# Kernel optimization log

Hardware: AMD Instinct MI355X
Metric: run time of the kernel (lower is better)

The kernel has to match this reference:

```python
import jax, jax.numpy as jnp
import numpy as np

N, E, F = 32768, 131072, 32

# (l_in, l_edge, l_out, op_type) for each of the 12 active paths; index = row of W
PATHS = [
    (0, 0, 0, 'prod'), (0, 1, 1, 'prod'), (0, 2, 2, 'prod'),
    (1, 0, 1, 'prod'), (2, 0, 2, 'prod'),
    (1, 1, 0, 'dot'), (1, 1, 1, 'cross'), (1, 1, 2, 'outer'),
    (2, 1, 1, 'mat_vec'), (1, 2, 1, 'vec_mat'),
    (2, 2, 0, 'double_dot'), (2, 2, 2, 'mat_mul_sym'),
]


def setup_inputs() -> dict:
    key = jax.random.key(0)
    ks = jax.random.split(key, 8)
    return {
        'h0': jax.random.normal(ks[0], (N, F), jnp.float32),
        'h1': jax.random.normal(ks[1], (N, 3, F), jnp.float32),
        'h2': jax.random.normal(ks[2], (N, 3, 3, F), jnp.float32),
        'g0': jax.random.normal(ks[3], (E, F), jnp.float32),
        'g1': jax.random.normal(ks[4], (E, 3, F), jnp.float32),
        'g2': jax.random.normal(ks[5], (E, 3, 3, F), jnp.float32),
        'W': jax.random.normal(ks[6], (len(PATHS), F, F), jnp.float32) * (F ** -0.5),
        'src': jax.random.randint(ks[7], (E,), 0, N, jnp.int32).astype(jnp.int64),
    }


def _leibniz(h0, h1, h2, g0, g1, g2, W, src):
    inv_sqrt_f = h0.shape[-1] ** -0.5
    # gather source-node features once per l
    h = {0: h0[src], 1: h1[src], 2: h2[src]}
    g = {0: g0, 1: g1, 2: g2}
    eye = jnp.eye(3, dtype=h0.dtype)[None, :, :, None]  # [1,3,3,1]
    msgs = {0: [], 1: [], 2: []}
    for p, (li, le, lo, op) in enumerate(PATHS):
        # nn.Linear(F,F,bias=False): y = x @ W^T, applied on last (feature) axis
        ht = jnp.einsum('...f,gf->...g', h[li], W[p])
        geom = g[le]
        if op == 'prod':
            if li == 0 and le == 0:
                res = ht * geom
            elif li == 0 and le == 1:
                res = ht[:, None, :] * geom
            elif li == 0 and le == 2:
                res = ht[:, None, None, :] * geom
            elif li == 1 and le == 0:
                res = ht * geom[:, None, :]
            else:  # li == 2, le == 0
                res = ht * geom[:, None, None, :]
        elif op == 'dot':
            res = jnp.sum(ht * geom, axis=1)
        elif op == 'cross':
            res = jnp.cross(ht, geom, axisa=1, axisb=1, axisc=1)
        elif op == 'outer':
            outer = ht[:, :, None, :] * geom[:, None, :, :]  # [E,3,3,F]
            trace = jnp.einsum('eiif->ef', outer)
            res = outer - (1.0 / 3.0) * trace[:, None, None, :] * eye
        elif op == 'mat_vec':
            res = jnp.einsum('eijf,ejf->eif', ht, geom)
        elif op == 'vec_mat':
            res = jnp.einsum('eif,eijf->ejf', ht, geom)
        elif op == 'double_dot':
            res = jnp.sum(ht * geom, axis=(1, 2))
        else:  # mat_mul_sym
            raw = jnp.einsum('eikf,ekjf->eijf', ht, geom)
            sym = 0.5 * (raw + jnp.swapaxes(raw, 1, 2))
            trace = jnp.einsum('eiif->ef', sym)
            res = sym - (1.0 / 3.0) * trace[:, None, None, :] * eye
        msgs[lo].append(res * inv_sqrt_f)
    return tuple(sum(msgs[l]) for l in (0, 1, 2))


def reference(h0, h1, h2, g0, g1, g2, W, src):
    return _leibniz(h0, h1, h2, g0, g1, g2, W, src)
```

## Files before the change

kernel.cpp:

```cpp
#include <hip/hip_runtime.h>

typedef float f32x4 __attribute__((ext_vector_type(4)));
typedef __bf16 bf16x8 __attribute__((ext_vector_type(8)));
typedef __bf16 bf16x4 __attribute__((ext_vector_type(4)));

constexpr float INV_SQRT_F = 0.17677669529663687f;

__device__ __forceinline__ f32x4 mfma16(bf16x8 a, bf16x8 b) {
  const f32x4 z = {0.f, 0.f, 0.f, 0.f};
  return __builtin_amdgcn_mfma_f32_16x16x32_bf16(a, b, z, 0, 0, 0);
}
__device__ __forceinline__ f32x4 ld4(const float* p) {
  return *reinterpret_cast<const f32x4*>(p);
}
__device__ __forceinline__ bf16x8 ldb8(const __bf16* __restrict__ p) {
  return *reinterpret_cast<const bf16x8*>(p);
}
__device__ __forceinline__ bf16x8 cvt_frag(f32x4 u, f32x4 v) {
  bf16x8 r;
  r[0] = (__bf16)u[0]; r[1] = (__bf16)u[1]; r[2] = (__bf16)u[2]; r[3] = (__bf16)u[3];
  r[4] = (__bf16)v[0]; r[5] = (__bf16)v[1]; r[6] = (__bf16)v[2]; r[7] = (__bf16)v[3];
  return r;
}

__global__ __launch_bounds__(256)
void leibniz_prepass(const float* __restrict__ h0, const float* __restrict__ h1,
                     const float* __restrict__ h2, const float* __restrict__ Wg,
                     __bf16* __restrict__ ws, int n0, int n1, int n2)
{
  if (blockIdx.x == 0) {
    bf16x8* wsW = reinterpret_cast<bf16x8*>(ws);
    for (int c = threadIdx.x; c < 12 * 2 * 4 * 16; c += 256) {
      const int gl = c & 15;
      const int qq = (c >> 4) & 3;
      const int hf = (c >> 6) & 1;
      const int p  = c >> 7;
      const float* wp = Wg + (p * 32 + hf * 16 + gl) * 32 + qq * 8;
      bf16x8 f;
#pragma unroll
      for (int j = 0; j < 8; ++j) f[j] = (__bf16)(wp[j] * INV_SQRT_F);
      wsW[c] = f;
    }
  }
  __bf16* hb0 = ws + 12288;
  __bf16* hb1 = hb0 + n0;
  __bf16* hb2 = hb1 + n1;
  const int q0 = n0 >> 2, q1 = n1 >> 2, q2 = n2 >> 2;
  const int total = q0 + q1 + q2;
  for (int i = blockIdx.x * 256 + threadIdx.x; i < total; i += gridDim.x * 256) {
    const float* sp;
    __bf16* dp;
    if (i < q0)           { sp = h0 + 4 * i;              dp = hb0 + 4 * i; }
    else if (i < q0 + q1) { int j = i - q0;      sp = h1 + 4 * j; dp = hb1 + 4 * j; }
    else                  { int j = i - q0 - q1; sp = h2 + 4 * j; dp = hb2 + 4 * j; }
    const f32x4 v = *reinterpret_cast<const f32x4*>(sp);
    bf16x4 o;
    o[0] = (__bf16)v[0]; o[1] = (__bf16)v[1]; o[2] = (__bf16)v[2]; o[3] = (__bf16)v[3];
    *reinterpret_cast<bf16x4*>(dp) = o;
  }
}

__global__ __launch_bounds__(256, 2)
void leibniz_half(const __bf16* __restrict__ wsAll,
                  const float* __restrict__ g0, const float* __restrict__ g1,
                  const float* __restrict__ g2, const int* __restrict__ src,
                  float* __restrict__ out, int E, int n0, int n1)
{
  __shared__ bf16x8 wlds[12 * 2 * 4 * 16];
  {
    const bf16x8* wsW = reinterpret_cast<const bf16x8*>(wsAll);
    for (int c = threadIdx.x; c < 12 * 2 * 4 * 16; c += 256) wlds[c] = wsW[c];
  }
  __syncthreads();

  const __bf16* hb0 = wsAll + 12288;
  const __bf16* hb1 = hb0 + n0;
  const __bf16* hb2 = hb1 + n1;

  const int lane = threadIdx.x & 63;
  const int wid  = threadIdx.x >> 6;
  const int half = wid & 1;
  const int tile = wid >> 1;
  const int eidx = lane & 15;
  const int q    = lane >> 4;
  int e0 = (blockIdx.x * 2 + tile) * 16;
  if (e0 > E - 16) e0 = E - 16;

  const int node = src[e0 + eidx];
  const int e    = e0 + eidx;
  const int col  = q * 4 + 16 * half;

  const float* g0p = g0 + (long long)e * 32 + col;
  const float* g1p = g1 + (long long)e * 96 + col;
  const float* g2p = g2 + (long long)e * 288 + col;
  const f32x4 gv0 = ld4(g0p);
  f32x4 gv1[3];
#pragma unroll
  for (int s = 0; s < 3; ++s) gv1[s] = ld4(g1p + s * 32);
  f32x4 gk[9];
#pragma unroll
  for (int s = 0; s < 9; ++s) gk[s] = ld4(g2p + s * 32);

  const int k0 = q * 8;
  const bf16x8 b0 = ldb8(hb0 + (long long)node * 32 + k0);
  bf16x8 b1[3];
#pragma unroll
  for (int s = 0; s < 3; ++s) b1[s] = ldb8(hb1 + (long long)node * 96 + s * 32 + k0);
  bf16x8 b2[9];
#pragma unroll
  for (int s = 0; s < 9; ++s) b2[s] = ldb8(hb2 + (long long)node * 288 + s * 32 + k0);

#define WFRAG(P) (wlds[(((P) * 2 + half) * 4 + q) * 16 + eidx])

  f32x4 acc0 = mfma16(WFRAG(0), b0) * gv0;
  f32x4 acc1[3];
  f32x4 acc2[9];
  {
    const bf16x8 w3 = WFRAG(3);
#pragma unroll
    for (int s = 0; s < 3; ++s) acc1[s] = mfma16(w3, b1[s]) * gv0;
    const bf16x8 w4 = WFRAG(4);
#pragma unroll
    for (int s = 0; s < 9; ++s) acc2[s] = mfma16(w4, b2[s]) * gv0;
  }

  {
    const f32x4 t = mfma16(WFRAG(1), b0);
#pragma unroll
    for (int s = 0; s < 3; ++s) acc1[s] += t * gv1[s];
  }
  {
    const bf16x8 w5 = WFRAG(5);
#pragma unroll
    for (int s = 0; s < 3; ++s) acc0 += mfma16(w5, b1[s]) * gv1[s];
  }
  {
    const bf16x8 w6 = WFRAG(6);
    const f32x4 c0 = mfma16(w6, b1[0]);
    const f32x4 c1 = mfma16(w6, b1[1]);
    const f32x4 c2 = mfma16(w6, b1[2]);
    acc1[0] += c1 * gv1[2] - c2 * gv1[1];
    acc1[1] += c2 * gv1[0] - c0 * gv1[2];
    acc1[2] += c0 * gv1[1] - c1 * gv1[0];
  }
  {
    const bf16x8 w7 = WFRAG(7);
    const f32x4 o0 = mfma16(w7, b1[0]);
    const f32x4 o1 = mfma16(w7, b1[1]);
    const f32x4 o2 = mfma16(w7, b1[2]);
    const f32x4 tr3 = (o0 * gv1[0] + o1 * gv1[1] + o2 * gv1[2]) * (1.f / 3.f);
    acc2[0] += o0 * gv1[0] - tr3;
    acc2[1] += o0 * gv1[1];
    acc2[2] += o0 * gv1[2];
    acc2[3] += o1 * gv1[0];
    acc2[4] += o1 * gv1[1] - tr3;
    acc2[5] += o1 * gv1[2];
    acc2[6] += o2 * gv1[0];
    acc2[7] += o2 * gv1[1];
    acc2[8] += o2 * gv1[2] - tr3;
  }
  {
    const bf16x8 w8 = WFRAG(8);
#pragma unroll
    for (int a = 0; a < 3; ++a)
#pragma unroll
      for (int b = 0; b < 3; ++b)
        acc1[a] += mfma16(w8, b2[a * 3 + b]) * gv1[b];
  }

  {
    const f32x4 t2 = mfma16(WFRAG(2), b0);
#pragma unroll
    for (int ss = 0; ss < 9; ++ss) acc2[ss] += t2 * gk[ss];
  }
  {
    const bf16x8 w9 = WFRAG(9);
#pragma unroll
    for (int i = 0; i < 3; ++i) {
      const f32x4 vk = mfma16(w9, b1[i]);
#pragma unroll
      for (int j = 0; j < 3; ++j) acc1[j] += vk * gk[i * 3 + j];
    }
  }
  {
    const bf16x8 w10 = WFRAG(10);
#pragma unroll
    for (int ss = 0; ss < 9; ++ss) acc0 += mfma16(w10, b2[ss]) * gk[ss];
  }
  {
    const bf16x8 w11 = WFRAG(11);
#pragma unroll
    for (int k = 0; k < 3; ++k) {
      const f32x4 m0 = mfma16(w11, b2[0 * 3 + k]);
      const f32x4 m1 = mfma16(w11, b2[1 * 3 + k]);
      const f32x4 m2 = mfma16(w11, b2[2 * 3 + k]);
      const f32x4 gk0 = gk[k * 3 + 0];
      const f32x4 gk1 = gk[k * 3 + 1];
      const f32x4 gk2 = gk[k * 3 + 2];
      const f32x4 tk3 = (m0 * gk0 + m1 * gk1 + m2 * gk2) * (1.f / 3.f);
      acc2[0] += m0 * gk0 - tk3;
      acc2[4] += m1 * gk1 - tk3;
      acc2[8] += m2 * gk2 - tk3;
      const f32x4 s01 = (m0 * gk1 + m1 * gk0) * 0.5f;
      acc2[1] += s01; acc2[3] += s01;
      const f32x4 s02 = (m0 * gk2 + m2 * gk0) * 0.5f;
      acc2[2] += s02; acc2[6] += s02;
      const f32x4 s12 = (m1 * gk2 + m2 * gk1) * 0.5f;
      acc2[5] += s12; acc2[7] += s12;
    }
  }

  __builtin_amdgcn_s_barrier();

  float* o0p = out + (long long)e * 32 + col;
  float* o1p = out + (long long)E * 32 + (long long)e * 96 + col;
  float* o2p = out + (long long)E * 128 + (long long)e * 288 + col;
  *reinterpret_cast<f32x4*>(o0p) = acc0;
#pragma unroll
  for (int s = 0; s < 3; ++s) *reinterpret_cast<f32x4*>(o1p + s * 32) = acc1[s];
#pragma unroll
  for (int s = 0; s < 9; ++s) *reinterpret_cast<f32x4*>(o2p + s * 32) = acc2[s];
#undef WFRAG
}

__device__ __forceinline__ bf16x8 load_frag8(const float* __restrict__ p) {
  return cvt_frag(ld4(p), ld4(p + 4));
}
__device__ __forceinline__ f32x4 ntload4(const float* __restrict__ p) {
  return __builtin_nontemporal_load(reinterpret_cast<const f32x4*>(p));
}
__device__ __forceinline__ void ntstore4(float* __restrict__ p, f32x4 v) {
  __builtin_nontemporal_store(v, reinterpret_cast<f32x4*>(p));
}

__global__ __launch_bounds__(256, 2)
void leibniz_fused(const float* __restrict__ h0, const float* __restrict__ h1,
                   const float* __restrict__ h2, const float* __restrict__ g0,
                   const float* __restrict__ g1, const float* __restrict__ g2,
                   const float* __restrict__ Wg, const int* __restrict__ src,
                   float* __restrict__ out, int E)
{
  __shared__ bf16x8 wlds[12 * 2 * 4 * 16];
  for (int c = threadIdx.x; c < 12 * 2 * 4 * 16; c += 256) {
    const int gl = c & 15;
    const int qq = (c >> 4) & 3;
    const int hf = (c >> 6) & 1;
    const int p  = c >> 7;
    const float* wp = Wg + (p * 32 + hf * 16 + gl) * 32 + qq * 8;
    bf16x8 f;
#pragma unroll
    for (int j = 0; j < 8; ++j) f[j] = (__bf16)(wp[j] * INV_SQRT_F);
    wlds[c] = f;
  }
  __syncthreads();

  const int lane = threadIdx.x & 63;
  const int wid  = threadIdx.x >> 6;
  const int eidx = lane & 15;
  const int q    = lane >> 4;
  int e0 = (blockIdx.x * 4 + wid) * 16;
  if (e0 > E - 16) e0 = E - 16;

  const int node = src[e0 + eidx];
  const int e   = e0 + eidx;
  const int col = q * 4;
  const float* g0p = g0 + e * 32 + col;
  const float* g1p = g1 + (long long)e * 96 + col;
  const float* g2p = g2 + (long long)e * 288 + col;

  f32x4 gv0[2];
  gv0[0] = ntload4(g0p); gv0[1] = ntload4(g0p + 16);
  f32x4 gv1[3][2];
#pragma unroll
  for (int s = 0; s < 3; ++s) {
    gv1[s][0] = ntload4(g1p + s * 32);
    gv1[s][1] = ntload4(g1p + s * 32 + 16);
  }

  const int k0 = q * 8;
  const bf16x8 b0 = load_frag8(h0 + node * 32 + k0);
  bf16x8 b1[3];
#pragma unroll
  for (int s = 0; s < 3; ++s) b1[s] = load_frag8(h1 + node * 96 + s * 32 + k0);
  bf16x8 b2[9];
#pragma unroll
  for (int s = 0; s < 9; ++s) b2[s] = load_frag8(h2 + node * 288 + s * 32 + k0);

  const f32x4 z4 = {0.f, 0.f, 0.f, 0.f};
  f32x4 acc0[2] = {z4, z4};
  f32x4 acc1[3][2];
  f32x4 acc2[9][2];
#pragma unroll
  for (int s = 0; s < 3; ++s) { acc1[s][0] = z4; acc1[s][1] = z4; }
#pragma unroll
  for (int s = 0; s < 9; ++s) { acc2[s][0] = z4; acc2[s][1] = z4; }

#define WFRAG(P, H) (wlds[(((P) * 2 + (H)) * 4 + q) * 16 + eidx])
#pragma unroll
  for (int h = 0; h < 2; ++h) {
    acc0[h] += mfma16(WFRAG(0, h), b0) * gv0[h];
    const bf16x8 w3 = WFRAG(3, h);
#pragma unroll
    for (int s = 0; s < 3; ++s) acc1[s][h] += mfma16(w3, b1[s]) * gv0[h];
    const bf16x8 w4 = WFRAG(4, h);
#pragma unroll
    for (int s = 0; s < 9; ++s) acc2[s][h] += mfma16(w4, b2[s]) * gv0[h];
  }

  f32x4 gkA[3][2];
#pragma unroll
  for (int j = 0; j < 3; ++j) {
    gkA[j][0] = ntload4(g2p + j * 32);
    gkA[j][1] = ntload4(g2p + j * 32 + 16);
  }

#pragma unroll
  for (int h = 0; h < 2; ++h) {
    {
      const f32x4 t = mfma16(WFRAG(1, h), b0);
#pragma unroll
      for (int s = 0; s < 3; ++s) acc1[s][h] += t * gv1[s][h];
    }
    {
      const bf16x8 w5 = WFRAG(5, h);
#pragma unroll
      for (int s = 0; s < 3; ++s) acc0[h] += mfma16(w5, b1[s]) * gv1[s][h];
    }
    {
      const bf16x8 w6 = WFRAG(6, h);
      const f32x4 c0 = mfma16(w6, b1[0]);
      const f32x4 c1 = mfma16(w6, b1[1]);
      const f32x4 c2 = mfma16(w6, b1[2]);
      acc1[0][h] += c1 * gv1[2][h] - c2 * gv1[1][h];
      acc1[1][h] += c2 * gv1[0][h] - c0 * gv1[2][h];
      acc1[2][h] += c0 * gv1[1][h] - c1 * gv1[0][h];
    }
    {
      const bf16x8 w7 = WFRAG(7, h);
      const f32x4 o0 = mfma16(w7, b1[0]);
      const f32x4 o1 = mfma16(w7, b1[1]);
      const f32x4 o2 = mfma16(w7, b1[2]);
      const f32x4 tr3 = (o0 * gv1[0][h] + o1 * gv1[1][h] + o2 * gv1[2][h]) * (1.f / 3.f);
      acc2[0][h] += o0 * gv1[0][h] - tr3;
      acc2[1][h] += o0 * gv1[1][h];
      acc2[2][h] += o0 * gv1[2][h];
      acc2[3][h] += o1 * gv1[0][h];
      acc2[4][h] += o1 * gv1[1][h] - tr3;
      acc2[5][h] += o1 * gv1[2][h];
      acc2[6][h] += o2 * gv1[0][h];
      acc2[7][h] += o2 * gv1[1][h];
      acc2[8][h] += o2 * gv1[2][h] - tr3;
    }
    {
      const bf16x8 w8 = WFRAG(8, h);
#pragma unroll
      for (int a = 0; a < 3; ++a)
#pragma unroll
        for (int b = 0; b < 3; ++b)
          acc1[a][h] += mfma16(w8, b2[a * 3 + b]) * gv1[b][h];
    }
  }

  f32x4 gkB[3][2];
#pragma unroll
  for (int j = 0; j < 3; ++j) {
    gkB[j][0] = ntload4(g2p + (3 + j) * 32);
    gkB[j][1] = ntload4(g2p + (3 + j) * 32 + 16);
  }

  f32x4 t2[2];
  t2[0] = mfma16(WFRAG(2, 0), b0);
  t2[1] = mfma16(WFRAG(2, 1), b0);

#define G2ROW_COMPUTE(K, GK)                                                   \
  {                                                                            \
    _Pragma("unroll")                                                          \
    for (int h = 0; h < 2; ++h) {                                              \
      _Pragma("unroll")                                                        \
      for (int j = 0; j < 3; ++j) acc2[(K) * 3 + j][h] += t2[h] * GK[j][h];    \
      {                                                                        \
        const f32x4 vk = mfma16(WFRAG(9, h), b1[(K)]);                         \
        _Pragma("unroll")                                                      \
        for (int j = 0; j < 3; ++j) acc1[j][h] += vk * GK[j][h];               \
      }                                                                        \
      {                                                                        \
        const bf16x8 w10 = WFRAG(10, h);                                       \
        _Pragma("unroll")                                                      \
        for (int j = 0; j < 3; ++j)                                            \
          acc0[h] += mfma16(w10, b2[(K) * 3 + j]) * GK[j][h];                  \
      }                                                                        \
      {                                                                        \
        const bf16x8 w11 = WFRAG(11, h);                                       \
        const f32x4 m0 = mfma16(w11, b2[0 * 3 + (K)]);                         \
        const f32x4 m1 = mfma16(w11, b2[1 * 3 + (K)]);                         \
        const f32x4 m2 = mfma16(w11, b2[2 * 3 + (K)]);                         \
        const f32x4 tk3 =                                                      \
            (m0 * GK[0][h] + m1 * GK[1][h] + m2 * GK[2][h]) * (1.f / 3.f);     \
        acc2[0][h] += m0 * GK[0][h] - tk3;                                     \
        acc2[4][h] += m1 * GK[1][h] - tk3;                                     \
        acc2[8][h] += m2 * GK[2][h] - tk3;                                     \
        const f32x4 s01 = (m0 * GK[1][h] + m1 * GK[0][h]) * 0.5f;              \
        acc2[1][h] += s01; acc2[3][h] += s01;                                  \
        const f32x4 s02 = (m0 * GK[2][h] + m2 * GK[0][h]) * 0.5f;              \
        acc2[2][h] += s02; acc2[6][h] += s02;                                  \
        const f32x4 s12 = (m1 * GK[2][h] + m2 * GK[1][h]) * 0.5f;              \
        acc2[5][h] += s12; acc2[7][h] += s12;                                  \
      }                                                                        \
    }                                                                          \
  }

  G2ROW_COMPUTE(0, gkA)
#pragma unroll
  for (int j = 0; j < 3; ++j) {
    gkA[j][0] = ntload4(g2p + (6 + j) * 32);
    gkA[j][1] = ntload4(g2p + (6 + j) * 32 + 16);
  }
  G2ROW_COMPUTE(1, gkB)
  G2ROW_COMPUTE(2, gkA)
#undef G2ROW_COMPUTE

  float* o0p = out + (long long)e * 32 + col;
  float* o1p = out + (long long)E * 32 + (long long)e * 96 + col;
  float* o2p = out + (long long)E * 128 + (long long)e * 288 + col;
  ntstore4(o0p, acc0[0]);
  ntstore4(o0p + 16, acc0[1]);
#pragma unroll
  for (int s = 0; s < 3; ++s) {
    ntstore4(o1p + s * 32, acc1[s][0]);
    ntstore4(o1p + s * 32 + 16, acc1[s][1]);
  }
#pragma unroll
  for (int s = 0; s < 9; ++s) {
    ntstore4(o2p + s * 32, acc2[s][0]);
    ntstore4(o2p + s * 32 + 16, acc2[s][1]);
  }
#undef WFRAG
}

extern "C" void kernel_launch(void* const* d_in, const int* in_sizes, int n_in,
                              void* d_out, int out_size, void* d_ws, size_t ws_size,
                              hipStream_t stream) {
  const float* h0 = (const float*)d_in[0];
  const float* h1 = (const float*)d_in[1];
  const float* h2 = (const float*)d_in[2];
  const float* g0 = (const float*)d_in[3];
  const float* g1 = (const float*)d_in[4];
  const float* g2 = (const float*)d_in[5];
  const float* Wg = (const float*)d_in[6];
  const int* src = (const int*)d_in[7];
  const int E = in_sizes[7];
  const int n0 = in_sizes[0], n1 = in_sizes[1], n2 = in_sizes[2];

  const size_t need = 24576 + (size_t)(n0 + n1 + n2) * 2;
  if (ws_size >= need) {
    __bf16* ws = (__bf16*)d_ws;
    leibniz_prepass<<<2048, 256, 0, stream>>>(h0, h1, h2, Wg, ws, n0, n1, n2);
    leibniz_half<<<(E + 31) / 32, 256, 0, stream>>>(ws, g0, g1, g2, src,
                                                    (float*)d_out, E, n0, n1);
  } else {
    leibniz_fused<<<(E + 63) / 64, 256, 0, stream>>>(h0, h1, h2, g0, g1, g2,
                                                     Wg, src, (float*)d_out, E);
  }
}
```

Before: 141.1 us.

## Make edge kernel persistent with register-resident weight fragments

Replaces the one-block-per-32-edges launch with a persistent grid of up to 1024 blocks that loop over edge tile pairs. The weight fragments are loaded once per thread into registers instead of being staged through LDS with a block barrier. This removes per-block startup costs and the shared-memory weight reads. In exchange it adds 12 bf16x8 registers per thread, which raises register pressure and may lower occupancy, and the loop no longer lets many blocks overlap their loads and stores.

```diff
diff --git a/kernel.cpp b/kernel.cpp
--- a/kernel.cpp
+++ b/kernel.cpp
@@ -61,166 +61,161 @@
 }
 
 __global__ __launch_bounds__(256, 2)
-void leibniz_half(const __bf16* __restrict__ wsAll,
-                  const float* __restrict__ g0, const float* __restrict__ g1,
-                  const float* __restrict__ g2, const int* __restrict__ src,
-                  float* __restrict__ out, int E, int n0, int n1)
+void leibniz_persist(const __bf16* __restrict__ wsAll,
+                     const float* __restrict__ g0, const float* __restrict__ g1,
+                     const float* __restrict__ g2, const int* __restrict__ src,
+                     float* __restrict__ out, int E, int n0, int n1)
 {
-  __shared__ bf16x8 wlds[12 * 2 * 4 * 16];
+  const int lane  = threadIdx.x & 63;
+  const int wid   = threadIdx.x >> 6;
+  const int half  = wid & 1;
+  const int tpair = wid >> 1;
+  const int eidx  = lane & 15;
+  const int q     = lane >> 4;
+  const int col   = q * 4 + 16 * half;
+
+  bf16x8 w[12];
   {
     const bf16x8* wsW = reinterpret_cast<const bf16x8*>(wsAll);
-    for (int c = threadIdx.x; c < 12 * 2 * 4 * 16; c += 256) wlds[c] = wsW[c];
-  }
-  __syncthreads();
-
+#pragma unroll
+    for (int p = 0; p < 12; ++p) w[p] = wsW[(p * 2 + half) * 64 + q * 16 + eidx];
+  }
   const __bf16* hb0 = wsAll + 12288;
   const __bf16* hb1 = hb0 + n0;
   const __bf16* hb2 = hb1 + n1;
 
-  const int lane = threadIdx.x & 63;
-  const int wid  = threadIdx.x >> 6;
-  const int half = wid & 1;
-  const int tile = wid >> 1;
-  const int eidx = lane & 15;
-  const int q    = lane >> 4;
-  int e0 = (blockIdx.x * 2 + tile) * 16;
-  if (e0 > E - 16) e0 = E - 16;
-
-  const int node = src[e0 + eidx];
-  const int e    = e0 + eidx;
-  const int col  = q * 4 + 16 * half;
-
-  const float* g0p = g0 + (long long)e * 32 + col;
-  const float* g1p = g1 + (long long)e * 96 + col;
-  const float* g2p = g2 + (long long)e * 288 + col;
-  const f32x4 gv0 = ld4(g0p);
-  f32x4 gv1[3];
-#pragma unroll
-  for (int s = 0; s < 3; ++s) gv1[s] = ld4(g1p + s * 32);
-  f32x4 gk[9];
-#pragma unroll
-  for (int s = 0; s < 9; ++s) gk[s] = ld4(g2p + s * 32);
-
-  const int k0 = q * 8;
-  const bf16x8 b0 = ldb8(hb0 + (long long)node * 32 + k0);
-  bf16x8 b1[3];
-#pragma unroll
-  for (int s = 0; s < 3; ++s) b1[s] = ldb8(hb1 + (long long)node * 96 + s * 32 + k0);
-  bf16x8 b2[9];
-#pragma unroll
-  for (int s = 0; s < 9; ++s) b2[s] = ldb8(hb2 + (long long)node * 288 + s * 32 + k0);
-
-#define WFRAG(P) (wlds[(((P) * 2 + half) * 4 + q) * 16 + eidx])
-
-  f32x4 acc0 = mfma16(WFRAG(0), b0) * gv0;
-  f32x4 acc1[3];
-  f32x4 acc2[9];
-  {
-    const bf16x8 w3 = WFRAG(3);
-#pragma unroll
-    for (int s = 0; s < 3; ++s) acc1[s] = mfma16(w3, b1[s]) * gv0;
-    const bf16x8 w4 = WFRAG(4);
-#pragma unroll
-    for (int s = 0; s < 9; ++s) acc2[s] = mfma16(w4, b2[s]) * gv0;
-  }
-
-  {
-    const f32x4 t = mfma16(WFRAG(1), b0);
-#pragma unroll
-    for (int s = 0; s < 3; ++s) acc1[s] += t * gv1[s];
-  }
-  {
-    const bf16x8 w5 = WFRAG(5);
-#pragma unroll
-    for (int s = 0; s < 3; ++s) acc0 += mfma16(w5, b1[s]) * gv1[s];
-  }
-  {
-    const bf16x8 w6 = WFRAG(6);
-    const f32x4 c0 = mfma16(w6, b1[0]);
-    const f32x4 c1 = mfma16(w6, b1[1]);
-    const f32x4 c2 = mfma16(w6, b1[2]);
-    acc1[0] += c1 * gv1[2] - c2 * gv1[1];
-    acc1[1] += c2 * gv1[0] - c0 * gv1[2];
-    acc1[2] += c0 * gv1[1] - c1 * gv1[0];
-  }
-  {
-    const bf16x8 w7 = WFRAG(7);
-    const f32x4 o0 = mfma16(w7, b1[0]);
-    const f32x4 o1 = mfma16(w7, b1[1]);
-    const f32x4 o2 = mfma16(w7, b1[2]);
-    const f32x4 tr3 = (o0 * gv1[0] + o1 * gv1[1] + o2 * gv1[2]) * (1.f / 3.f);
-    acc2[0] += o0 * gv1[0] - tr3;
-    acc2[1] += o0 * gv1[1];
-    acc2[2] += o0 * gv1[2];
-    acc2[3] += o1 * gv1[0];
-    acc2[4] += o1 * gv1[1] - tr3;
-    acc2[5] += o1 * gv1[2];
-    acc2[6] += o2 * gv1[0];
-    acc2[7] += o2 * gv1[1];
-    acc2[8] += o2 * gv1[2] - tr3;
-  }
-  {
-    const bf16x8 w8 = WFRAG(8);
-#pragma unroll
-    for (int a = 0; a < 3; ++a)
-#pragma unroll
-      for (int b = 0; b < 3; ++b)
-        acc1[a] += mfma16(w8, b2[a * 3 + b]) * gv1[b];
-  }
-
-  {
-    const f32x4 t2 = mfma16(WFRAG(2), b0);
-#pragma unroll
-    for (int ss = 0; ss < 9; ++ss) acc2[ss] += t2 * gk[ss];
-  }
-  {
-    const bf16x8 w9 = WFRAG(9);
-#pragma unroll
-    for (int i = 0; i < 3; ++i) {
-      const f32x4 vk = mfma16(w9, b1[i]);
-#pragma unroll
-      for (int j = 0; j < 3; ++j) acc1[j] += vk * gk[i * 3 + j];
-    }
-  }
-  {
-    const bf16x8 w10 = WFRAG(10);
-#pragma unroll
-    for (int ss = 0; ss < 9; ++ss) acc0 += mfma16(w10, b2[ss]) * gk[ss];
-  }
-  {
-    const bf16x8 w11 = WFRAG(11);
-#pragma unroll
-    for (int k = 0; k < 3; ++k) {
-      const f32x4 m0 = mfma16(w11, b2[0 * 3 + k]);
-      const f32x4 m1 = mfma16(w11, b2[1 * 3 + k]);
-      const f32x4 m2 = mfma16(w11, b2[2 * 3 + k]);
-      const f32x4 gk0 = gk[k * 3 + 0];
-      const f32x4 gk1 = gk[k * 3 + 1];
-      const f32x4 gk2 = gk[k * 3 + 2];
-      const f32x4 tk3 = (m0 * gk0 + m1 * gk1 + m2 * gk2) * (1.f / 3.f);
-      acc2[0] += m0 * gk0 - tk3;
-      acc2[4] += m1 * gk1 - tk3;
-      acc2[8] += m2 * gk2 - tk3;
-      const f32x4 s01 = (m0 * gk1 + m1 * gk0) * 0.5f;
-      acc2[1] += s01; acc2[3] += s01;
-      const f32x4 s02 = (m0 * gk2 + m2 * gk0) * 0.5f;
-      acc2[2] += s02; acc2[6] += s02;
-      const f32x4 s12 = (m1 * gk2 + m2 * gk1) * 0.5f;
-      acc2[5] += s12; acc2[7] += s12;
-    }
-  }
-
-  __builtin_amdgcn_s_barrier();
-
-  float* o0p = out + (long long)e * 32 + col;
-  float* o1p = out + (long long)E * 32 + (long long)e * 96 + col;
-  float* o2p = out + (long long)E * 128 + (long long)e * 288 + col;
-  *reinterpret_cast<f32x4*>(o0p) = acc0;
-#pragma unroll
-  for (int s = 0; s < 3; ++s) *reinterpret_cast<f32x4*>(o1p + s * 32) = acc1[s];
-#pragma unroll
-  for (int s = 0; s < 9; ++s) *reinterpret_cast<f32x4*>(o2p + s * 32) = acc2[s];
-#undef WFRAG
+  const int NT   = (E + 15) >> 4;
+  const int NT2  = (NT + 1) >> 1;
+  const int nb   = gridDim.x;
+  const int iters = (NT2 + nb - 1) / nb;
+  const long long o1base = (long long)E * 32;
+  const long long o2base = (long long)E * 128;
+
+  for (int it = 0; it < iters; ++it) {
+    const int tp = blockIdx.x + it * nb;
+    int tile = tp * 2 + tpair;
+    const bool active = tile < NT;
+    if (active) {
+      long long e0 = (long long)tile * 16;
+      if (e0 > E - 16) e0 = E - 16;
+      const int node = src[e0 + eidx];
+      const long long e = e0 + eidx;
+
+      const float* g0p = g0 + e * 32 + col;
+      const float* g1p = g1 + e * 96 + col;
+      const float* g2p = g2 + e * 288 + col;
+      const f32x4 gv0 = ld4(g0p);
+      f32x4 gv1[3];
+#pragma unroll
+      for (int s = 0; s < 3; ++s) gv1[s] = ld4(g1p + s * 32);
+      f32x4 gk[9];
+#pragma unroll
+      for (int s = 0; s < 9; ++s) gk[s] = ld4(g2p + s * 32);
+
+      const int k0 = q * 8;
+      const bf16x8 b0 = ldb8(hb0 + (long long)node * 32 + k0);
+      bf16x8 b1[3];
+#pragma unroll
+      for (int s = 0; s < 3; ++s)
+        b1[s] = ldb8(hb1 + (long long)node * 96 + s * 32 + k0);
+      bf16x8 b2[9];
+#pragma unroll
+      for (int s = 0; s < 9; ++s)
+        b2[s] = ldb8(hb2 + (long long)node * 288 + s * 32 + k0);
+
+      f32x4 acc0 = mfma16(w[0], b0) * gv0;
+      f32x4 acc1[3];
+      f32x4 acc2[9];
+#pragma unroll
+      for (int s = 0; s < 3; ++s) acc1[s] = mfma16(w[3], b1[s]) * gv0;
+#pragma unroll
+      for (int s = 0; s < 9; ++s) acc2[s] = mfma16(w[4], b2[s]) * gv0;
+
+      {
+        const f32x4 t = mfma16(w[1], b0);
+#pragma unroll
+        for (int s = 0; s < 3; ++s) acc1[s] += t * gv1[s];
+      }
+#pragma unroll
+      for (int s = 0; s < 3; ++s) acc0 += mfma16(w[5], b1[s]) * gv1[s];
+      {
+        const f32x4 c0 = mfma16(w[6], b1[0]);
+        const f32x4 c1 = mfma16(w[6], b1[1]);
+        const f32x4 c2 = mfma16(w[6], b1[2]);
+        acc1[0] += c1 * gv1[2] - c2 * gv1[1];
+        acc1[1] += c2 * gv1[0] - c0 * gv1[2];
+        acc1[2] += c0 * gv1[1] - c1 * gv1[0];
+      }
+      {
+        const f32x4 o0 = mfma16(w[7], b1[0]);
+        const f32x4 o1 = mfma16(w[7], b1[1]);
+        const f32x4 o2 = mfma16(w[7], b1[2]);
+        const f32x4 tr3 = (o0 * gv1[0] + o1 * gv1[1] + o2 * gv1[2]) * (1.f / 3.f);
+        acc2[0] += o0 * gv1[0] - tr3;
+        acc2[1] += o0 * gv1[1];
+        acc2[2] += o0 * gv1[2];
+        acc2[3] += o1 * gv1[0];
+        acc2[4] += o1 * gv1[1] - tr3;
+        acc2[5] += o1 * gv1[2];
+        acc2[6] += o2 * gv1[0];
+        acc2[7] += o2 * gv1[1];
+        acc2[8] += o2 * gv1[2] - tr3;
+      }
+#pragma unroll
+      for (int a = 0; a < 3; ++a)
+#pragma unroll
+        for (int b = 0; b < 3; ++b)
+          acc1[a] += mfma16(w[8], b2[a * 3 + b]) * gv1[b];
+
+      {
+        const f32x4 t2 = mfma16(w[2], b0);
+#pragma unroll
+        for (int ss = 0; ss < 9; ++ss) acc2[ss] += t2 * gk[ss];
+      }
+#pragma unroll
+      for (int i = 0; i < 3; ++i) {
+        const f32x4 vk = mfma16(w[9], b1[i]);
+#pragma unroll
+        for (int j = 0; j < 3; ++j) acc1[j] += vk * gk[i * 3 + j];
+      }
+#pragma unroll
+      for (int ss = 0; ss < 9; ++ss) acc0 += mfma16(w[10], b2[ss]) * gk[ss];
+#pragma unroll
+      for (int k = 0; k < 3; ++k) {
+        const f32x4 m0 = mfma16(w[11], b2[0 * 3 + k]);
+        const f32x4 m1 = mfma16(w[11], b2[1 * 3 + k]);
+        const f32x4 m2 = mfma16(w[11], b2[2 * 3 + k]);
+        const f32x4 gk0 = gk[k * 3 + 0];
+        const f32x4 gk1 = gk[k * 3 + 1];
+        const f32x4 gk2 = gk[k * 3 + 2];
+        const f32x4 tk3 = (m0 * gk0 + m1 * gk1 + m2 * gk2) * (1.f / 3.f);
+        acc2[0] += m0 * gk0 - tk3;
+        acc2[4] += m1 * gk1 - tk3;
+        acc2[8] += m2 * gk2 - tk3;
+        const f32x4 s01 = (m0 * gk1 + m1 * gk0) * 0.5f;
+        acc2[1] += s01; acc2[3] += s01;
+        const f32x4 s02 = (m0 * gk2 + m2 * gk0) * 0.5f;
+        acc2[2] += s02; acc2[6] += s02;
+        const f32x4 s12 = (m1 * gk2 + m2 * gk1) * 0.5f;
+        acc2[5] += s12; acc2[7] += s12;
+      }
+
+      __builtin_amdgcn_s_barrier();
+
+      float* o0p = out + e * 32 + col;
+      float* o1p = out + o1base + e * 96 + col;
+      float* o2p = out + o2base + e * 288 + col;
+      *reinterpret_cast<f32x4*>(o0p) = acc0;
+#pragma unroll
+      for (int s = 0; s < 3; ++s)
+        *reinterpret_cast<f32x4*>(o1p + s * 32) = acc1[s];
+#pragma unroll
+      for (int s = 0; s < 9; ++s)
+        *reinterpret_cast<f32x4*>(o2p + s * 32) = acc2[s];
+    } else {
+      __builtin_amdgcn_s_barrier();
+    }
+  }
 }
 
 __device__ __forceinline__ bf16x8 load_frag8(const float* __restrict__ p) {
@@ -455,8 +450,12 @@
   if (ws_size >= need) {
     __bf16* ws = (__bf16*)d_ws;
     leibniz_prepass<<<2048, 256, 0, stream>>>(h0, h1, h2, Wg, ws, n0, n1, n2);
-    leibniz_half<<<(E + 31) / 32, 256, 0, stream>>>(ws, g0, g1, g2, src,
-                                                    (float*)d_out, E, n0, n1);
+    const int NT  = (E + 15) / 16;
+    const int NT2 = (NT + 1) / 2;
+    int blocks = 1024;
+    if (blocks > NT2) blocks = NT2;
+    leibniz_persist<<<blocks, 256, 0, stream>>>(ws, g0, g1, g2, src,
+                                                (float*)d_out, E, n0, n1);
   } else {
     leibniz_fused<<<(E + 63) / 64, 256, 0, stream>>>(h0, h1, h2, g0, g1, g2,
                                                      Wg, src, (float*)d_out, E);
```

After: 150.9 us. 1.07x slower.
